# Kernel optimization log

Measured on AMD Instinct MI355X. Metric: run time of the kernel, lower is better.

Reference implementation:

```python
import jax, jax.numpy as jnp
import numpy as np

N_GENES = 768
HID = 128


def setup_inputs() -> dict:
    key = jax.random.key(0)
    ks = jax.random.split(key, 7)
    s1 = 1.0 / np.sqrt(2 * HID)
    s2 = 1.0 / np.sqrt(HID)
    return {
        "gene_embeddings": jax.random.normal(ks[0], (N_GENES, HID), jnp.float32),
        # regulatory_classifier: Linear(2h -> h), ReLU, Linear(h -> 3)
        "W1": jax.random.normal(ks[1], (HID, 2 * HID), jnp.float32) * s1,
        "b1": jax.random.normal(ks[2], (HID,), jnp.float32) * s1,
        "W2": jax.random.normal(ks[3], (3, HID), jnp.float32) * s2,
        "b2": jax.random.normal(ks[4], (3,), jnp.float32) * s2,
        # binding_predictor: Bilinear(h, h, 1) -> weight [1, h, h], bias [1]
        "Wb": jax.random.normal(ks[5], (1, HID, HID), jnp.float32) * s2,
        "bb": jax.random.normal(ks[6], (1,), jnp.float32) * s2,
    }


def reference(gene_embeddings, W1, b1, W2, b2, Wb, bb):
    """Vectorized equivalent of GeneRegulatoryNetwork.compute_regulatory_matrix.

    For every ordered pair (i, j), i != j:
      logits   = MLP(cat[x_i, x_j])            -> [3]
      cls      = argmax(logits)
      affinity = x_i^T Wb x_j + bb             (nn.Bilinear, out=1)
      reg[i,j] = +affinity if cls==0, -affinity if cls==2, else 0
    """
    X = gene_embeddings  # [n, h]
    n, h = X.shape
    # Linear(2h -> h) on cat[x_i, x_j] splits into two per-gene projections.
    Ai = X @ W1[:, :h].T  # [n, h] contribution of gene_i
    Bj = X @ W1[:, h:].T  # [n, h] contribution of gene_j
    hidden = jax.nn.relu(Ai[:, None, :] + Bj[None, :, :] + b1)  # [n, n, h]
    logits = hidden @ W2.T + b2  # [n, n, 3]
    reg_class = jnp.argmax(logits, axis=-1)  # [n, n] (first-max, matches torch)
    # Bilinear affinity: x_i^T Wb[0] x_j + bb[0]
    affinity = jnp.einsum('ik,kl,jl->ij', X, Wb[0], X) + bb[0]  # [n, n]
    sign = jnp.where(reg_class == 0, 1.0, jnp.where(reg_class == 2, -1.0, 0.0))
    reg = (sign * affinity).astype(X.dtype)
    # i == j pairs are skipped in the original loop -> zero diagonal
    reg = reg * (1.0 - jnp.eye(n, dtype=reg.dtype))
    return reg
```

## Files before the change

kernel.cpp:

```cpp
#include <hip/hip_runtime.h>

#define N_GENES 768
#define H 128
#define TILE 48
#define LDP 132
#define LDPH 136

typedef float    f2 __attribute__((ext_vector_type(2)));
typedef _Float16 h2 __attribute__((ext_vector_type(2)));
typedef _Float16 h8 __attribute__((ext_vector_type(8)));

__global__ __launch_bounds__(128) void grn_pre(
    const float* __restrict__ X, const float* __restrict__ W1,
    const float* __restrict__ b1, const float* __restrict__ Wb,
    const float* __restrict__ W2,
    float* __restrict__ AiB, float* __restrict__ Bjp, float* __restrict__ Wd,
    _Float16* __restrict__ Yh, _Float16* __restrict__ Xh)
{
    const int m  = threadIdx.x;
    const int g0 = blockIdx.x * 3;

    __shared__ float Xs[3][H];
    #pragma unroll
    for (int r = 0; r < 3; ++r) Xs[r][m] = X[(g0 + r) * H + m];
    __syncthreads();

    double aib[3] = {0, 0, 0}, bj[3] = {0, 0, 0}, y[3] = {0, 0, 0};
    const float4* W1a = (const float4*)(W1 + m * (2 * H));
    const float4* W1b = (const float4*)(W1 + m * (2 * H) + H);

    #pragma unroll 4
    for (int kq = 0; kq < H / 4; ++kq) {
        float4 wa = W1a[kq];
        float4 wb = W1b[kq];
        float wc[4];
        #pragma unroll
        for (int e = 0; e < 4; ++e) wc[e] = Wb[(kq * 4 + e) * H + m];
        const float* wae = &wa.x;
        const float* wbe = &wb.x;
        #pragma unroll
        for (int r = 0; r < 3; ++r) {
            float4 xr = *(const float4*)&Xs[r][kq * 4];
            const float* xe = &xr.x;
            #pragma unroll
            for (int e = 0; e < 4; ++e) {
                aib[r] += (double)xe[e] * (double)wae[e];
                bj[r]  += (double)xe[e] * (double)wbe[e];
                y[r]   += (double)xe[e] * (double)wc[e];
            }
        }
    }

    const double b1m = (double)b1[m];
    #pragma unroll
    for (int r = 0; r < 3; ++r) {
        AiB[(g0 + r) * H + m] = (float)(aib[r] + b1m);
        Bjp[(g0 + r) * H + m] = (float)bj[r];
        Yh [(g0 + r) * H + m] = (_Float16)(float)y[r];
        Xh [(g0 + r) * H + m] = (_Float16)Xs[r][m];
    }

    if (blockIdx.x == 0) {
        Wd[2 * m]     = W2[m] - W2[2 * H + m];
        Wd[2 * m + 1] = W2[m] - W2[H + m];
    }
}

__device__ __forceinline__ void load_tile_f32(float* __restrict__ dst,
                                              const float* __restrict__ src, int tx)
{
    #pragma unroll
    for (int t = 0; t < 6; ++t) {
        int idx = tx + t * 256;
        int row = idx >> 5;
        int c4  = idx & 31;
        *(float4*)&dst[row * LDP + c4 * 4] = *(const float4*)&src[row * H + c4 * 4];
    }
}

__device__ __forceinline__ void load_tile_f16(_Float16* __restrict__ dst,
                                              const _Float16* __restrict__ src, int tx)
{
    #pragma unroll
    for (int t = 0; t < 3; ++t) {
        int idx = tx + t * 256;
        int row = idx >> 4;
        int c8  = idx & 15;
        *(h8*)&dst[row * LDPH + c8 * 8] = *(const h8*)&src[row * H + c8 * 8];
    }
}

__device__ __forceinline__ h2 hpair(h8 v, int p) { h2 r; r.x = v[2*p]; r.y = v[2*p+1]; return r; }

__global__ __launch_bounds__(256) void grn_main(
    const float* __restrict__ AiB, const float* __restrict__ Bjp,
    const _Float16* __restrict__ Yh, const _Float16* __restrict__ Xh,
    const float* __restrict__ Wd,  const float* __restrict__ b2,
    const float* __restrict__ bb,  float* __restrict__ out)
{
    const int gj = blockIdx.x & 15;
    const int gi = blockIdx.x >> 4;
    const int tx = threadIdx.x;
    const int it = tx >> 4;
    const int jt = tx & 15;

    __shared__ _Float16 sLh[TILE * LDPH];
    __shared__ _Float16 sRh[TILE * LDPH];
    __shared__ float    sR [TILE * LDP];

    load_tile_f16(sLh, Yh + gi * TILE * H, tx);
    load_tile_f16(sRh, Xh + gj * TILE * H, tx);
    load_tile_f32(sR,  Bjp + gj * TILE * H, tx);
    __syncthreads();

    float aff[3][3] = {};
    #pragma unroll 2
    for (int q = 0; q < H / 8; ++q) {
        h8 yv[3], xv[3];
        #pragma unroll
        for (int r = 0; r < 3; ++r) yv[r] = *(const h8*)&sLh[(it + 16 * r) * LDPH + q * 8];
        #pragma unroll
        for (int c = 0; c < 3; ++c) xv[c] = *(const h8*)&sRh[(jt + 16 * c) * LDPH + q * 8];
        #pragma unroll
        for (int r = 0; r < 3; ++r)
            #pragma unroll
            for (int c = 0; c < 3; ++c)
                #pragma unroll
                for (int p = 0; p < 4; ++p) {
#if __has_builtin(__builtin_amdgcn_fdot2)
                    aff[r][c] = __builtin_amdgcn_fdot2(hpair(yv[r], p), hpair(xv[c], p),
                                                       aff[r][c], false);
#else
                    h2 a = hpair(yv[r], p), b = hpair(xv[c], p);
                    aff[r][c] = fmaf((float)a.x, (float)b.x, aff[r][c]);
                    aff[r][c] = fmaf((float)a.y, (float)b.y, aff[r][c]);
#endif
                }
    }

    const f2 uv0 = {b2[0] - b2[2], b2[0] - b2[1]};
    f2 uv[3][3];
    #pragma unroll
    for (int r = 0; r < 3; ++r)
        #pragma unroll
        for (int c = 0; c < 3; ++c) uv[r][c] = uv0;

    const float* aRow = AiB + (gi * TILE + it) * H;
    const float4* Wduv = (const float4*)Wd;

    const f2 zero2 = {0.0f, 0.0f};
    #pragma unroll 4
    for (int mq = 0; mq < H / 4; ++mq) {
        float4 wq0 = Wduv[2 * mq];
        float4 wq1 = Wduv[2 * mq + 1];
        float4 av[3], bv[3];
        #pragma unroll
        for (int r = 0; r < 3; ++r) av[r] = *(const float4*)(aRow + r * 16 * H + mq * 4);
        #pragma unroll
        for (int c = 0; c < 3; ++c) bv[c] = *(const float4*)&sR[(jt + 16 * c) * LDP + mq * 4];
        #pragma unroll
        for (int r = 0; r < 3; ++r) {
            f2 a01 = {av[r].x, av[r].y};
            f2 a23 = {av[r].z, av[r].w};
            #pragma unroll
            for (int c = 0; c < 3; ++c) {
                f2 b01 = {bv[c].x, bv[c].y};
                f2 b23 = {bv[c].z, bv[c].w};
                f2 h01 = __builtin_elementwise_max(a01 + b01, zero2);
                f2 h23 = __builtin_elementwise_max(a23 + b23, zero2);
                f2 t = uv[r][c];
                t = (f2){h01.x, h01.x} * (f2){wq0.x, wq0.y} + t;
                t = (f2){h01.y, h01.y} * (f2){wq0.z, wq0.w} + t;
                t = (f2){h23.x, h23.x} * (f2){wq1.x, wq1.y} + t;
                t = (f2){h23.y, h23.y} * (f2){wq1.z, wq1.w} + t;
                uv[r][c] = t;
            }
        }
    }

    const float bbv = bb[0];
    #pragma unroll
    for (int r = 0; r < 3; ++r) {
        const int i = gi * TILE + it + 16 * r;
        #pragma unroll
        for (int c = 0; c < 3; ++c) {
            const int j = gj * TILE + jt + 16 * c;
            float A = aff[r][c] + bbv;
            float uu = uv[r][c].x, vv = uv[r][c].y;
            float s = (uu >= 0.0f && vv >= 0.0f) ? A
                    : ((uu < 0.0f && uu < vv) ? -A : 0.0f);
            if (i == j) s = 0.0f;
            out[i * N_GENES + j] = s;
        }
    }
}

extern "C" void kernel_launch(void* const* d_in, const int* in_sizes, int n_in,
                              void* d_out, int out_size, void* d_ws, size_t ws_size,
                              hipStream_t stream)
{
    const float* X  = (const float*)d_in[0];
    const float* W1 = (const float*)d_in[1];
    const float* b1 = (const float*)d_in[2];
    const float* W2 = (const float*)d_in[3];
    const float* b2 = (const float*)d_in[4];
    const float* Wb = (const float*)d_in[5];
    const float* bb = (const float*)d_in[6];
    float* out = (float*)d_out;

    float* ws = (float*)d_ws;
    float*    AiB = ws;
    float*    Bjp = ws + N_GENES * H;
    float*    Wd  = ws + 2 * N_GENES * H;
    _Float16* Yh  = (_Float16*)(ws + 2 * N_GENES * H + 256);
    _Float16* Xh  = Yh + N_GENES * H;

    grn_pre <<<N_GENES / 3, 128, 0, stream>>>(X, W1, b1, Wb, W2, AiB, Bjp, Wd, Yh, Xh);
    grn_main<<<256,         256, 0, stream>>>(AiB, Bjp, Yh, Xh, Wd, b2, bb, out);
}
```

Before: 90.45 us.

## Shrink main-kernel tile to 48x16 and launch more blocks

The main kernel now gives each block 48 rows by 16 columns instead of 48x48, so the grid grows from 256 to 768 blocks and each thread owns 3 outputs instead of 9. The Y half-precision rows and the AiB rows are read straight from global memory rather than staged in shared memory, and only the small column tiles are put in LDS. The goal is to fill more of the MI355X's compute units and raise occupancy. The cost is less register-level reuse per thread and more global traffic for the row operands.

```diff
diff --git a/kernel.cpp b/kernel.cpp
--- a/kernel.cpp
+++ b/kernel.cpp
@@ -2,7 +2,8 @@
 
 #define N_GENES 768
 #define H 128
-#define TILE 48
+#define TI 48
+#define TJ 16
 #define LDP 132
 #define LDPH 136
 
@@ -66,86 +67,61 @@
     }
 }
 
-__device__ __forceinline__ void load_tile_f32(float* __restrict__ dst,
-                                              const float* __restrict__ src, int tx)
-{
-    #pragma unroll
-    for (int t = 0; t < 6; ++t) {
-        int idx = tx + t * 256;
-        int row = idx >> 5;
-        int c4  = idx & 31;
-        *(float4*)&dst[row * LDP + c4 * 4] = *(const float4*)&src[row * H + c4 * 4];
-    }
-}
-
-__device__ __forceinline__ void load_tile_f16(_Float16* __restrict__ dst,
-                                              const _Float16* __restrict__ src, int tx)
-{
-    #pragma unroll
-    for (int t = 0; t < 3; ++t) {
-        int idx = tx + t * 256;
-        int row = idx >> 4;
-        int c8  = idx & 15;
-        *(h8*)&dst[row * LDPH + c8 * 8] = *(const h8*)&src[row * H + c8 * 8];
-    }
-}
-
-__device__ __forceinline__ h2 hpair(h8 v, int p) { h2 r; r.x = v[2*p]; r.y = v[2*p+1]; return r; }
-
 __global__ __launch_bounds__(256) void grn_main(
     const float* __restrict__ AiB, const float* __restrict__ Bjp,
     const _Float16* __restrict__ Yh, const _Float16* __restrict__ Xh,
     const float* __restrict__ Wd,  const float* __restrict__ b2,
     const float* __restrict__ bb,  float* __restrict__ out)
 {
-    const int gj = blockIdx.x & 15;
-    const int gi = blockIdx.x >> 4;
+    const int gj = blockIdx.x % 48;
+    const int gi = blockIdx.x / 48;
     const int tx = threadIdx.x;
     const int it = tx >> 4;
     const int jt = tx & 15;
 
-    __shared__ _Float16 sLh[TILE * LDPH];
-    __shared__ _Float16 sRh[TILE * LDPH];
-    __shared__ float    sR [TILE * LDP];
+    __shared__ _Float16 sXh[TJ * LDPH];
+    __shared__ float    sB [TJ * LDP];
 
-    load_tile_f16(sLh, Yh + gi * TILE * H, tx);
-    load_tile_f16(sRh, Xh + gj * TILE * H, tx);
-    load_tile_f32(sR,  Bjp + gj * TILE * H, tx);
+    {
+        int row = tx >> 4, c8 = tx & 15;
+        *(h8*)&sXh[row * LDPH + c8 * 8] =
+            *(const h8*)&Xh[(gj * TJ + row) * H + c8 * 8];
+        #pragma unroll
+        for (int t = 0; t < 2; ++t) {
+            int k  = tx + t * 256;
+            int r2 = k >> 5, c4 = k & 31;
+            *(float4*)&sB[r2 * LDP + c4 * 4] =
+                *(const float4*)&Bjp[(gj * TJ + r2) * H + c4 * 4];
+        }
+    }
     __syncthreads();
 
-    float aff[3][3] = {};
-    #pragma unroll 2
+    float aff[3] = {0.0f, 0.0f, 0.0f};
+    const _Float16* yRow = Yh + (gi * TI + it) * H;
+    #pragma unroll 4
     for (int q = 0; q < H / 8; ++q) {
-        h8 yv[3], xv[3];
+        h8 xv = *(const h8*)&sXh[jt * LDPH + q * 8];
+        h8 yv[3];
         #pragma unroll
-        for (int r = 0; r < 3; ++r) yv[r] = *(const h8*)&sLh[(it + 16 * r) * LDPH + q * 8];
-        #pragma unroll
-        for (int c = 0; c < 3; ++c) xv[c] = *(const h8*)&sRh[(jt + 16 * c) * LDPH + q * 8];
+        for (int r = 0; r < 3; ++r) yv[r] = *(const h8*)(yRow + r * 16 * H + q * 8);
         #pragma unroll
         for (int r = 0; r < 3; ++r)
             #pragma unroll
-            for (int c = 0; c < 3; ++c)
-                #pragma unroll
-                for (int p = 0; p < 4; ++p) {
+            for (int p = 0; p < 4; ++p) {
+                h2 a; a.x = yv[r][2*p]; a.y = yv[r][2*p+1];
+                h2 b; b.x = xv[2*p];    b.y = xv[2*p+1];
 #if __has_builtin(__builtin_amdgcn_fdot2)
-                    aff[r][c] = __builtin_amdgcn_fdot2(hpair(yv[r], p), hpair(xv[c], p),
-                                                       aff[r][c], false);
+                aff[r] = __builtin_amdgcn_fdot2(a, b, aff[r], false);
 #else
-                    h2 a = hpair(yv[r], p), b = hpair(xv[c], p);
-                    aff[r][c] = fmaf((float)a.x, (float)b.x, aff[r][c]);
-                    aff[r][c] = fmaf((float)a.y, (float)b.y, aff[r][c]);
+                aff[r] = fmaf((float)a.x, (float)b.x, aff[r]);
+                aff[r] = fmaf((float)a.y, (float)b.y, aff[r]);
 #endif
-                }
+            }
     }
 
     const f2 uv0 = {b2[0] - b2[2], b2[0] - b2[1]};
-    f2 uv[3][3];
-    #pragma unroll
-    for (int r = 0; r < 3; ++r)
-        #pragma unroll
-        for (int c = 0; c < 3; ++c) uv[r][c] = uv0;
-
-    const float* aRow = AiB + (gi * TILE + it) * H;
+    f2 uv[3] = {uv0, uv0, uv0};
+    const float*  aRow = AiB + (gi * TI + it) * H;
     const float4* Wduv = (const float4*)Wd;
 
     const f2 zero2 = {0.0f, 0.0f};
@@ -153,45 +129,34 @@
     for (int mq = 0; mq < H / 4; ++mq) {
         float4 wq0 = Wduv[2 * mq];
         float4 wq1 = Wduv[2 * mq + 1];
-        float4 av[3], bv[3];
-        #pragma unroll
-        for (int r = 0; r < 3; ++r) av[r] = *(const float4*)(aRow + r * 16 * H + mq * 4);
-        #pragma unroll
-        for (int c = 0; c < 3; ++c) bv[c] = *(const float4*)&sR[(jt + 16 * c) * LDP + mq * 4];
+        float4 bv  = *(const float4*)&sB[jt * LDP + mq * 4];
+        f2 b01 = {bv.x, bv.y}, b23 = {bv.z, bv.w};
         #pragma unroll
         for (int r = 0; r < 3; ++r) {
-            f2 a01 = {av[r].x, av[r].y};
-            f2 a23 = {av[r].z, av[r].w};
-            #pragma unroll
-            for (int c = 0; c < 3; ++c) {
-                f2 b01 = {bv[c].x, bv[c].y};
-                f2 b23 = {bv[c].z, bv[c].w};
-                f2 h01 = __builtin_elementwise_max(a01 + b01, zero2);
-                f2 h23 = __builtin_elementwise_max(a23 + b23, zero2);
-                f2 t = uv[r][c];
-                t = (f2){h01.x, h01.x} * (f2){wq0.x, wq0.y} + t;
-                t = (f2){h01.y, h01.y} * (f2){wq0.z, wq0.w} + t;
-                t = (f2){h23.x, h23.x} * (f2){wq1.x, wq1.y} + t;
-                t = (f2){h23.y, h23.y} * (f2){wq1.z, wq1.w} + t;
-                uv[r][c] = t;
-            }
+            float4 av = *(const float4*)(aRow + r * 16 * H + mq * 4);
+            f2 a01 = {av.x, av.y}, a23 = {av.z, av.w};
+            f2 h01 = __builtin_elementwise_max(a01 + b01, zero2);
+            f2 h23 = __builtin_elementwise_max(a23 + b23, zero2);
+            f2 t = uv[r];
+            t = (f2){h01.x, h01.x} * (f2){wq0.x, wq0.y} + t;
+            t = (f2){h01.y, h01.y} * (f2){wq0.z, wq0.w} + t;
+            t = (f2){h23.x, h23.x} * (f2){wq1.x, wq1.y} + t;
+            t = (f2){h23.y, h23.y} * (f2){wq1.z, wq1.w} + t;
+            uv[r] = t;
         }
     }
 
     const float bbv = bb[0];
+    const int j = gj * TJ + jt;
     #pragma unroll
     for (int r = 0; r < 3; ++r) {
-        const int i = gi * TILE + it + 16 * r;
-        #pragma unroll
-        for (int c = 0; c < 3; ++c) {
-            const int j = gj * TILE + jt + 16 * c;
-            float A = aff[r][c] + bbv;
-            float uu = uv[r][c].x, vv = uv[r][c].y;
-            float s = (uu >= 0.0f && vv >= 0.0f) ? A
-                    : ((uu < 0.0f && uu < vv) ? -A : 0.0f);
-            if (i == j) s = 0.0f;
-            out[i * N_GENES + j] = s;
-        }
+        const int i = gi * TI + it + 16 * r;
+        float A = aff[r] + bbv;
+        float uu = uv[r].x, vv = uv[r].y;
+        float s = (uu >= 0.0f && vv >= 0.0f) ? A
+                : ((uu < 0.0f && uu < vv) ? -A : 0.0f);
+        if (i == j) s = 0.0f;
+        out[i * N_GENES + j] = s;
     }
 }
 
@@ -216,5 +181,5 @@
     _Float16* Xh  = Yh + N_GENES * H;
 
     grn_pre <<<N_GENES / 3, 128, 0, stream>>>(X, W1, b1, Wb, W2, AiB, Bjp, Wd, Yh, Xh);
-    grn_main<<<256,         256, 0, stream>>>(AiB, Bjp, Yh, Xh, Wd, b2, bb, out);
+    grn_main<<<16 * 48,     256, 0, stream>>>(AiB, Bjp, Yh, Xh, Wd, b2, bb, out);
 }
```

Result: no change. 91.36 us (+1.0%).
